# Kernel optimization log

Measured on AMD Instinct MI355X. Metric: run time of the kernel, lower is better.

## Reference

```python
import jax, jax.numpy as jnp
import numpy as np

N_NODES = 100000
N_EDGES = 800000
IN = 128
HID = 128
EMB = 64
OUT = 8
N_GRAPHS = 64


def setup_inputs() -> dict:
    key = jax.random.key(0)
    ks = jax.random.split(key, 12)
    x = jax.random.normal(ks[0], (N_NODES, IN), dtype=jnp.float32)
    edge_index = jax.random.randint(ks[1], (2, N_EDGES), 0, N_NODES, dtype=jnp.int64)
    batch = jnp.sort(jax.random.randint(ks[2], (N_NODES,), 0, N_GRAPHS, dtype=jnp.int64))
    embed = jax.random.normal(ks[3], (N_GRAPHS, EMB), dtype=jnp.float32)
    s_in = 1.0 / np.sqrt(IN).astype(np.float32)
    s_h = 1.0 / np.sqrt(HID).astype(np.float32)
    s_l = 1.0 / np.sqrt(HID + EMB).astype(np.float32)
    return {
        "x": x,
        "edge_index": edge_index,
        "batch": batch,
        "embed": embed,
        # SAGEConv1: out = lin_l(mean_agg) + lin_r(x); bias lives in lin_l
        "W1l": jax.random.normal(ks[4], (HID, IN), dtype=jnp.float32) * s_in,
        "b1l": jnp.zeros((HID,), dtype=jnp.float32),
        "W1r": jax.random.normal(ks[5], (HID, IN), dtype=jnp.float32) * s_in,
        # SAGEConv2
        "W2l": jax.random.normal(ks[6], (HID, HID), dtype=jnp.float32) * s_h,
        "b2l": jnp.zeros((HID,), dtype=jnp.float32),
        "W2r": jax.random.normal(ks[7], (HID, HID), dtype=jnp.float32) * s_h,
        # final Linear(hidden + embed_dim, out)
        "Wlin": jax.random.normal(ks[8], (OUT, HID + EMB), dtype=jnp.float32) * s_l,
        "blin": jnp.zeros((OUT,), dtype=jnp.float32),
    }


def _segment_mean(vals, idx, num_segments):
    # scatter-mean with count clamped to 1 (matches PyG scatter 'mean')
    s = jax.ops.segment_sum(vals, idx, num_segments=num_segments)
    c = jax.ops.segment_sum(jnp.ones((vals.shape[0], 1), vals.dtype), idx,
                            num_segments=num_segments)
    return s / jnp.maximum(c, 1.0)


def reference(x, edge_index, batch, embed, W1l, b1l, W1r, W2l, b2l, W2r, Wlin, blin):
    src, dst = edge_index[0], edge_index[1]

    def sage(h, Wl, bl, Wr):
        # gather source features, mean-aggregate at destination, then linear
        agg = _segment_mean(h[src], dst, N_NODES)          # [N, d]
        return agg @ Wl.T + bl + h @ Wr.T                   # [N, HID]

    h = jax.nn.relu(sage(x, W1l, b1l, W1r))
    h = jax.nn.relu(sage(h, W2l, b2l, W2r))
    pooled = _segment_mean(h, batch, N_GRAPHS)              # [G, HID]
    z = jnp.concatenate([pooled, embed], axis=1)            # [G, HID+EMB]
    return z @ Wlin.T + blin                                # [G, OUT]
```

## Files before the change

### kernel.cpp

```cpp
#include <hip/hip_runtime.h>
#include <stdint.h>

#define FEAT   128
#define GR     64
#define LDA    136
#define NBUCK  256
#define BSHIFT 9

typedef __attribute__((ext_vector_type(8))) short bf8_t;
typedef __attribute__((ext_vector_type(4))) float f4_t;

__device__ inline float bf2f(ushort h){
    union { uint u; float f; } v; v.u = ((uint)h) << 16; return v.f;
}
__device__ inline float bf2f_lo(uint u){
    union { uint u; float f; } v; v.u = u << 16; return v.f;
}
__device__ inline float bf2f_hi(uint u){
    union { uint u; float f; } v; v.u = u & 0xffff0000u; return v.f;
}
__device__ inline ushort f2bf(float f){
    union { float f; uint u; } v; v.f = f;
    uint r = (v.u + 0x7FFFu + ((v.u >> 16) & 1u)) >> 16;
    return (ushort)r;
}

__global__ void k_cast(const float* __restrict__ x, ushort* __restrict__ xb, int n4){
    int i = blockIdx.x * blockDim.x + threadIdx.x;
    if (i >= n4) return;
    float4 v = ((const float4*)x)[i];
    ushort4 o; o.x = f2bf(v.x); o.y = f2bf(v.y); o.z = f2bf(v.z); o.w = f2bf(v.w);
    ((ushort4*)xb)[i] = o;
}

__global__ void k_castw(const float* __restrict__ a0, const float* __restrict__ a1,
                        const float* __restrict__ a2, const float* __restrict__ a3,
                        ushort* __restrict__ o0, ushort* __restrict__ o1,
                        ushort* __restrict__ o2, ushort* __restrict__ o3){
    int i = blockIdx.x * blockDim.x + threadIdx.x;
    int sel = i >> 12, j = i & 4095;
    const float* s = sel == 0 ? a0 : sel == 1 ? a1 : sel == 2 ? a2 : a3;
    ushort*      d = sel == 0 ? o0 : sel == 1 ? o1 : sel == 2 ? o2 : o3;
    float4 v = ((const float4*)s)[j];
    ushort4 o; o.x = f2bf(v.x); o.y = f2bf(v.y); o.z = f2bf(v.z); o.w = f2bf(v.w);
    ((ushort4*)d)[j] = o;
}

__global__ void k_hist(const int* __restrict__ dst, int* __restrict__ bcnt, int E){
    __shared__ int h[NBUCK];
    h[threadIdx.x] = 0;
    __syncthreads();
    int base = blockIdx.x * 4096 + threadIdx.x;
    #pragma unroll
    for (int k = 0; k < 16; k++){
        int e = base + k * 256;
        if (e < E) atomicAdd(&h[dst[e] >> BSHIFT], 1);
    }
    __syncthreads();
    int c = h[threadIdx.x];
    if (c) atomicAdd(&bcnt[threadIdx.x], c);
}

__global__ void k_bscan(const int* __restrict__ bcnt, int* __restrict__ bbase,
                        int* __restrict__ bpos, int* __restrict__ rowp,
                        int* __restrict__ csr, int E, int M){
    __shared__ int sd[NBUCK];
    int t = threadIdx.x;
    int v = bcnt[t];
    sd[t] = v; __syncthreads();
    for (int off = 1; off < NBUCK; off <<= 1){
        int x = (t >= off) ? sd[t - off] : 0;
        __syncthreads();
        sd[t] += x;
        __syncthreads();
    }
    int ex = sd[t] - v;
    bbase[t] = ex;
    bpos[t]  = ex;
    if (t < 8) csr[E + t] = 0;
    if (t == NBUCK - 1){ bbase[NBUCK] = sd[t]; rowp[M] = E; }
}

__global__ __launch_bounds__(256) void k_bucket(const int* __restrict__ src,
                                                const int* __restrict__ dst,
                                                int* __restrict__ bpos,
                                                int2* __restrict__ bp, int E){
    __shared__ int h[NBUCK];
    __shared__ int bb[NBUCK];
    int t = threadIdx.x;
    h[t] = 0;
    __syncthreads();
    int base = blockIdx.x * 4096 + t;
    int bk[16], sv[16], dv[16];
    #pragma unroll
    for (int k = 0; k < 16; k++){
        int e = base + k * 256;
        if (e < E){
            dv[k] = dst[e]; sv[k] = src[e];
            bk[k] = dv[k] >> BSHIFT;
            atomicAdd(&h[bk[k]], 1);
        } else bk[k] = -1;
    }
    __syncthreads();
    int c = h[t];
    bb[t] = c ? atomicAdd(&bpos[t], c) : 0;
    __syncthreads();
    h[t] = 0;
    __syncthreads();
    #pragma unroll
    for (int k = 0; k < 16; k++){
        if (bk[k] >= 0){
            int r = atomicAdd(&h[bk[k]], 1);
            bp[bb[bk[k]] + r] = make_int2(sv[k], dv[k]);
        }
    }
}

__global__ __launch_bounds__(512) void k_csr(const int2* __restrict__ bp,
                                             const int* __restrict__ bbase,
                                             int* __restrict__ rowp,
                                             int* __restrict__ csr, int M){
    __shared__ int cnt[512];
    __shared__ int sd[512];
    int b = blockIdx.x, t = threadIdx.x;
    int nbase = b << BSHIFT;
    int nnodes = min(512, M - nbase);
    int e0 = bbase[b], e1 = bbase[b + 1];
    cnt[t] = 0;
    __syncthreads();
    for (int e = e0 + t; e < e1; e += 512)
        atomicAdd(&cnt[bp[e].y - nbase], 1);
    __syncthreads();
    int v = cnt[t];
    sd[t] = v; __syncthreads();
    for (int off = 1; off < 512; off <<= 1){
        int x = (t >= off) ? sd[t - off] : 0;
        __syncthreads();
        sd[t] += x;
        __syncthreads();
    }
    int ex = sd[t] - v;
    if (t < nnodes) rowp[nbase + t] = e0 + ex;
    cnt[t] = ex;
    __syncthreads();
    for (int e = e0 + t; e < e1; e += 512){
        int2 pr = bp[e];
        int r = atomicAdd(&cnt[pr.y - nbase], 1);
        csr[e0 + r] = pr.x;
    }
}

#define ACC4(vv)                                   \
    acc0 += bf2f_lo((vv).x); acc1 += bf2f_hi((vv).x); \
    acc2 += bf2f_lo((vv).y); acc3 += bf2f_hi((vv).y); \
    acc4 += bf2f_lo((vv).z); acc5 += bf2f_hi((vv).z); \
    acc6 += bf2f_lo((vv).w); acc7 += bf2f_hi((vv).w);

__global__ __launch_bounds__(256) void k_agg(const ushort* __restrict__ srcf,
                                             const int* __restrict__ rowp,
                                             const int* __restrict__ csr,
                                             ushort* __restrict__ aggb, int M){
    int node = blockIdx.x * 16 + (threadIdx.x >> 4);
    int l    = threadIdx.x & 15;
    if (node >= M) return;
    int s = rowp[node], e = rowp[node + 1];
    const char* base = (const char*)srcf + (uint)l * 16u;
    float acc0 = 0.f, acc1 = 0.f, acc2 = 0.f, acc3 = 0.f;
    float acc4 = 0.f, acc5 = 0.f, acc6 = 0.f, acc7 = 0.f;
    int i = s;
    for (; i + 4 <= e; i += 4){
        int idx[4];
        __builtin_memcpy(idx, csr + i, 16);
        uint4 v0 = *(const uint4*)(base + ((uint)idx[0] << 8));
        uint4 v1 = *(const uint4*)(base + ((uint)idx[1] << 8));
        uint4 v2 = *(const uint4*)(base + ((uint)idx[2] << 8));
        uint4 v3 = *(const uint4*)(base + ((uint)idx[3] << 8));
        ACC4(v0); ACC4(v1); ACC4(v2); ACC4(v3);
    }
    for (; i < e; i++){
        uint4 v = *(const uint4*)(base + ((uint)csr[i] << 8));
        ACC4(v);
    }
    float inv = (e > s) ? 1.0f / (float)(e - s) : 0.f;
    uint4 o;
    o.x = ((uint)f2bf(acc1 * inv) << 16) | (uint)f2bf(acc0 * inv);
    o.y = ((uint)f2bf(acc3 * inv) << 16) | (uint)f2bf(acc2 * inv);
    o.z = ((uint)f2bf(acc5 * inv) << 16) | (uint)f2bf(acc4 * inv);
    o.w = ((uint)f2bf(acc7 * inv) << 16) | (uint)f2bf(acc6 * inv);
    *(uint4*)(aggb + (size_t)node * FEAT + l * 8) = o;
}

__global__ __launch_bounds__(256) void k_gemm(
    const ushort* __restrict__ Aagg, const ushort* __restrict__ Aself,
    const ushort* __restrict__ Wl, const ushort* __restrict__ Wr,
    const float* __restrict__ bias, ushort* __restrict__ Hout, int M)
{
    __shared__ ushort As[64 * LDA];
    __shared__ ushort Bs[128 * LDA];
    const int tid  = threadIdx.x;
    const int lane = tid & 63;
    const int wave = tid >> 6;
    const int l15  = lane & 15;
    const int quad = lane >> 4;
    const int m0   = blockIdx.x * 64;

    f4_t acc[8];
    #pragma unroll
    for (int i = 0; i < 8; i++) acc[i] = (f4_t){0.f, 0.f, 0.f, 0.f};

    #pragma unroll
    for (int pass = 0; pass < 2; pass++){
        const ushort* Ap = pass ? Aself : Aagg;
        const ushort* Wp = pass ? Wr    : Wl;
        #pragma unroll
        for (int it = 0; it < 4; it++){
            int idx = (it * 256 + tid) * 8;
            int r = idx >> 7, c = idx & 127;
            int4 v = {0, 0, 0, 0};
            if (m0 + r < M) v = *(const int4*)(Ap + (size_t)(m0 + r) * FEAT + c);
            *(int4*)(&As[r * LDA + c]) = v;
        }
        #pragma unroll
        for (int it = 0; it < 8; it++){
            int idx = (it * 256 + tid) * 8;
            int r = idx >> 7, c = idx & 127;
            *(int4*)(&Bs[r * LDA + c]) = *(const int4*)(Wp + idx);
        }
        __syncthreads();
        const ushort* arow = &As[(wave * 16 + l15) * LDA + quad * 8];
        const ushort* brow = &Bs[l15 * LDA + quad * 8];
        #pragma unroll
        for (int nt = 0; nt < 8; nt++){
            #pragma unroll
            for (int ks = 0; ks < 4; ks++){
                bf8_t a = *(const bf8_t*)(arow + ks * 32);
                bf8_t b = *(const bf8_t*)(brow + nt * 16 * LDA + ks * 32);
                acc[nt] = __builtin_amdgcn_mfma_f32_16x16x32_bf16(a, b, acc[nt], 0, 0, 0);
            }
        }
        __syncthreads();
    }
    #pragma unroll
    for (int nt = 0; nt < 8; nt++){
        int col = nt * 16 + l15;
        float bcol = bias[col];
        #pragma unroll
        for (int reg = 0; reg < 4; reg++){
            int gm = m0 + wave * 16 + quad * 4 + reg;
            if (gm < M){
                float v = acc[nt][reg] + bcol;
                v = v > 0.f ? v : 0.f;
                Hout[(size_t)gm * FEAT + col] = f2bf(v);
            }
        }
    }
}

__global__ void k_pool(const ushort* __restrict__ h, const int* __restrict__ batch,
                       float* __restrict__ pooled, int M){
    int f   = threadIdx.x & 127;
    int sub = threadIdx.x >> 7;
    int n0  = (blockIdx.x * 2 + sub) * 16;
    if (n0 >= M) return;
    int n1 = min(n0 + 16, M);
    int g = batch[n0];
    float s = 0.f;
    int n = n0;
    for (; n + 4 <= n1; n += 4){
        int g0 = batch[n], g1 = batch[n + 1], g2 = batch[n + 2], g3 = batch[n + 3];
        float v0 = bf2f(h[(size_t)n * FEAT + f]);
        float v1 = bf2f(h[(size_t)(n + 1) * FEAT + f]);
        float v2 = bf2f(h[(size_t)(n + 2) * FEAT + f]);
        float v3 = bf2f(h[(size_t)(n + 3) * FEAT + f]);
        if (g0 != g){ atomicAdd(&pooled[g * FEAT + f], s); s = 0.f; g = g0; } s += v0;
        if (g1 != g){ atomicAdd(&pooled[g * FEAT + f], s); s = 0.f; g = g1; } s += v1;
        if (g2 != g){ atomicAdd(&pooled[g * FEAT + f], s); s = 0.f; g = g2; } s += v2;
        if (g3 != g){ atomicAdd(&pooled[g * FEAT + f], s); s = 0.f; g = g3; } s += v3;
    }
    for (; n < n1; n++){
        int gn = batch[n];
        if (gn != g){ atomicAdd(&pooled[g * FEAT + f], s); s = 0.f; g = gn; }
        s += bf2f(h[(size_t)n * FEAT + f]);
    }
    atomicAdd(&pooled[g * FEAT + f], s);
}

__global__ void k_final(const float* __restrict__ pooled, const int* __restrict__ batch,
                        const float* __restrict__ embed, const float* __restrict__ Wlin,
                        const float* __restrict__ blin, float* __restrict__ out, int M){
    int t = threadIdx.x;
    if (t >= GR * 8) return;
    int g = t >> 3, o = t & 7;
    int lo = 0, hi = M;
    while (lo < hi){ int mid = (lo + hi) >> 1; if (batch[mid] < g) lo = mid + 1; else hi = mid; }
    int s0 = lo;
    lo = s0; hi = M;
    while (lo < hi){ int mid = (lo + hi) >> 1; if (batch[mid] < g + 1) lo = mid + 1; else hi = mid; }
    int c = lo - s0;
    float inv = (c > 0) ? 1.0f / (float)c : 0.f;
    float acc = blin[o];
    const float* wr = Wlin + o * (FEAT + GR);
    for (int k = 0; k < FEAT; k++) acc += pooled[g * FEAT + k] * inv * wr[k];
    for (int k = 0; k < GR; k++)   acc += embed[g * GR + k] * wr[FEAT + k];
    out[g * 8 + o] = acc;
}

extern "C" void kernel_launch(void* const* d_in, const int* in_sizes, int n_in,
                              void* d_out, int out_size, void* d_ws, size_t ws_size,
                              hipStream_t stream)
{
    const float* x     = (const float*)d_in[0];
    const int*   eidx  = (const int*)d_in[1];
    const int*   batch = (const int*)d_in[2];
    const float* embed = (const float*)d_in[3];
    const float* W1l   = (const float*)d_in[4];
    const float* b1l   = (const float*)d_in[5];
    const float* W1r   = (const float*)d_in[6];
    const float* W2l   = (const float*)d_in[7];
    const float* b2l   = (const float*)d_in[8];
    const float* W2r   = (const float*)d_in[9];
    const float* Wlin  = (const float*)d_in[10];
    const float* blin  = (const float*)d_in[11];
    float* out = (float*)d_out;

    const int M = in_sizes[0] / FEAT;
    const int E = in_sizes[1] / 2;
    const int* src = eidx;
    const int* dst = eidx + E;

    char* w = (char*)d_ws;
    size_t off = 0;
    auto alloc = [&](size_t sz){ void* p = w + off; off = (off + sz + 255) & ~(size_t)255; return p; };
    ushort* xb     = (ushort*)alloc((size_t)M * FEAT * 2);
    ushort* aggb   = (ushort*)alloc((size_t)M * FEAT * 2);
    ushort* h1b    = (ushort*)alloc((size_t)M * FEAT * 2);
    int*    rowp   = (int*)alloc((size_t)(M + 1) * 4);
    int*    csr    = (int*)alloc((size_t)(E + 8) * 4);
    int*    bcnt   = (int*)alloc(NBUCK * 4);
    int*    bbase  = (int*)alloc((NBUCK + 1) * 4);
    int*    bpos   = (int*)alloc(NBUCK * 4);
    float*  pooled = (float*)alloc((size_t)GR * FEAT * 4);
    ushort* w1lb   = (ushort*)alloc((size_t)FEAT * FEAT * 2);
    ushort* w1rb   = (ushort*)alloc((size_t)FEAT * FEAT * 2);
    ushort* w2lb   = (ushort*)alloc((size_t)FEAT * FEAT * 2);
    ushort* w2rb   = (ushort*)alloc((size_t)FEAT * FEAT * 2);
    int2*   bp     = (int2*)aggb;
    ushort* h2b    = xb;

    hipMemsetAsync(bcnt, 0, NBUCK * 4, stream);
    hipMemsetAsync(pooled, 0, (size_t)GR * FEAT * 4, stream);

    const int nb   = (M + 511) >> BSHIFT;
    const int ebk  = (E + 4095) / 4096;
    k_cast  <<<(M * FEAT / 4 + 255) / 256, 256, 0, stream>>>(x, xb, M * FEAT / 4);
    k_castw <<<64, 256, 0, stream>>>(W1l, W1r, W2l, W2r, w1lb, w1rb, w2lb, w2rb);
    k_hist  <<<ebk, 256, 0, stream>>>(dst, bcnt, E);
    k_bscan <<<1, NBUCK, 0, stream>>>(bcnt, bbase, bpos, rowp, csr, E, M);
    k_bucket<<<ebk, 256, 0, stream>>>(src, dst, bpos, bp, E);
    k_csr   <<<nb, 512, 0, stream>>>(bp, bbase, rowp, csr, M);
    k_agg   <<<(M + 15) / 16, 256, 0, stream>>>(xb, rowp, csr, aggb, M);
    k_gemm  <<<(M + 63) / 64, 256, 0, stream>>>(aggb, xb, w1lb, w1rb, b1l, h1b, M);
    k_agg   <<<(M + 15) / 16, 256, 0, stream>>>(h1b, rowp, csr, aggb, M);
    k_gemm  <<<(M + 63) / 64, 256, 0, stream>>>(aggb, h1b, w2lb, w2rb, b2l, h2b, M);
    k_pool  <<<(M + 31) / 32, 256, 0, stream>>>(h2b, batch, pooled, M);
    k_final <<<1, 512, 0, stream>>>(pooled, batch, embed, Wlin, blin, out, M);
}
```

Measured before the change: 309.0 us.

## Fuse neighbor aggregation into SAGE GEMM kernel and read weights directly

Merges the gather-mean aggregation and the dual GEMM into one kernel per layer. Each block aggregates neighbors for its 64 rows straight into shared memory, loads self-features directly into registers, and reads weight fragments from global memory (L2-cached) instead of staging them in LDS. This removes the aggregated-feature buffer's write and re-read, plus two kernel launches per layer. In exchange, the gather phase now runs at the GEMM kernel's occupancy with one barrier before the MFMAs, and the weight loads are uncoalesced global reads.

```diff
diff --git a/kernel.cpp b/kernel.cpp
--- a/kernel.cpp
+++ b/kernel.cpp
@@ -156,47 +156,13 @@
     acc4 += bf2f_lo((vv).z); acc5 += bf2f_hi((vv).z); \
     acc6 += bf2f_lo((vv).w); acc7 += bf2f_hi((vv).w);
 
-__global__ __launch_bounds__(256) void k_agg(const ushort* __restrict__ srcf,
-                                             const int* __restrict__ rowp,
-                                             const int* __restrict__ csr,
-                                             ushort* __restrict__ aggb, int M){
-    int node = blockIdx.x * 16 + (threadIdx.x >> 4);
-    int l    = threadIdx.x & 15;
-    if (node >= M) return;
-    int s = rowp[node], e = rowp[node + 1];
-    const char* base = (const char*)srcf + (uint)l * 16u;
-    float acc0 = 0.f, acc1 = 0.f, acc2 = 0.f, acc3 = 0.f;
-    float acc4 = 0.f, acc5 = 0.f, acc6 = 0.f, acc7 = 0.f;
-    int i = s;
-    for (; i + 4 <= e; i += 4){
-        int idx[4];
-        __builtin_memcpy(idx, csr + i, 16);
-        uint4 v0 = *(const uint4*)(base + ((uint)idx[0] << 8));
-        uint4 v1 = *(const uint4*)(base + ((uint)idx[1] << 8));
-        uint4 v2 = *(const uint4*)(base + ((uint)idx[2] << 8));
-        uint4 v3 = *(const uint4*)(base + ((uint)idx[3] << 8));
-        ACC4(v0); ACC4(v1); ACC4(v2); ACC4(v3);
-    }
-    for (; i < e; i++){
-        uint4 v = *(const uint4*)(base + ((uint)csr[i] << 8));
-        ACC4(v);
-    }
-    float inv = (e > s) ? 1.0f / (float)(e - s) : 0.f;
-    uint4 o;
-    o.x = ((uint)f2bf(acc1 * inv) << 16) | (uint)f2bf(acc0 * inv);
-    o.y = ((uint)f2bf(acc3 * inv) << 16) | (uint)f2bf(acc2 * inv);
-    o.z = ((uint)f2bf(acc5 * inv) << 16) | (uint)f2bf(acc4 * inv);
-    o.w = ((uint)f2bf(acc7 * inv) << 16) | (uint)f2bf(acc6 * inv);
-    *(uint4*)(aggb + (size_t)node * FEAT + l * 8) = o;
-}
-
-__global__ __launch_bounds__(256) void k_gemm(
-    const ushort* __restrict__ Aagg, const ushort* __restrict__ Aself,
-    const ushort* __restrict__ Wl, const ushort* __restrict__ Wr,
-    const float* __restrict__ bias, ushort* __restrict__ Hout, int M)
+__global__ __launch_bounds__(256) void k_sage(
+    const ushort* __restrict__ Aself, const int* __restrict__ rowp,
+    const int* __restrict__ csr, const ushort* __restrict__ Wl,
+    const ushort* __restrict__ Wr, const float* __restrict__ bias,
+    ushort* __restrict__ Hout, int M)
 {
     __shared__ ushort As[64 * LDA];
-    __shared__ ushort Bs[128 * LDA];
     const int tid  = threadIdx.x;
     const int lane = tid & 63;
     const int wave = tid >> 6;
@@ -204,42 +170,80 @@
     const int quad = lane >> 4;
     const int m0   = blockIdx.x * 64;
 
+    int srowi = m0 + wave * 16 + l15;
+    if (srowi >= M) srowi = M - 1;
+    const ushort* srow = Aself + (size_t)srowi * FEAT + quad * 8;
+    bf8_t sa0 = *(const bf8_t*)(srow);
+    bf8_t sa1 = *(const bf8_t*)(srow + 32);
+    bf8_t sa2 = *(const bf8_t*)(srow + 64);
+    bf8_t sa3 = *(const bf8_t*)(srow + 96);
+
+    {
+        const int l   = tid & 15;
+        const int grp = tid >> 4;
+        const char* gbase = (const char*)Aself + (uint)l * 16u;
+        #pragma unroll
+        for (int p = 0; p < 4; p++){
+            int r = p * 16 + grp;
+            int node = m0 + r;
+            float acc0 = 0.f, acc1 = 0.f, acc2 = 0.f, acc3 = 0.f;
+            float acc4 = 0.f, acc5 = 0.f, acc6 = 0.f, acc7 = 0.f;
+            float inv = 0.f;
+            if (node < M){
+                int s = rowp[node], e = rowp[node + 1];
+                int i = s;
+                for (; i + 4 <= e; i += 4){
+                    int idx[4];
+                    __builtin_memcpy(idx, csr + i, 16);
+                    uint4 v0 = *(const uint4*)(gbase + ((uint)idx[0] << 8));
+                    uint4 v1 = *(const uint4*)(gbase + ((uint)idx[1] << 8));
+                    uint4 v2 = *(const uint4*)(gbase + ((uint)idx[2] << 8));
+                    uint4 v3 = *(const uint4*)(gbase + ((uint)idx[3] << 8));
+                    ACC4(v0); ACC4(v1); ACC4(v2); ACC4(v3);
+                }
+                for (; i < e; i++){
+                    uint4 v = *(const uint4*)(gbase + ((uint)csr[i] << 8));
+                    ACC4(v);
+                }
+                inv = (e > s) ? 1.0f / (float)(e - s) : 0.f;
+            }
+            uint4 o;
+            o.x = ((uint)f2bf(acc1 * inv) << 16) | (uint)f2bf(acc0 * inv);
+            o.y = ((uint)f2bf(acc3 * inv) << 16) | (uint)f2bf(acc2 * inv);
+            o.z = ((uint)f2bf(acc5 * inv) << 16) | (uint)f2bf(acc4 * inv);
+            o.w = ((uint)f2bf(acc7 * inv) << 16) | (uint)f2bf(acc6 * inv);
+            *(uint4*)(&As[r * LDA + l * 8]) = o;
+        }
+    }
+    __syncthreads();
+
     f4_t acc[8];
     #pragma unroll
     for (int i = 0; i < 8; i++) acc[i] = (f4_t){0.f, 0.f, 0.f, 0.f};
 
-    #pragma unroll
-    for (int pass = 0; pass < 2; pass++){
-        const ushort* Ap = pass ? Aself : Aagg;
-        const ushort* Wp = pass ? Wr    : Wl;
-        #pragma unroll
-        for (int it = 0; it < 4; it++){
-            int idx = (it * 256 + tid) * 8;
-            int r = idx >> 7, c = idx & 127;
-            int4 v = {0, 0, 0, 0};
-            if (m0 + r < M) v = *(const int4*)(Ap + (size_t)(m0 + r) * FEAT + c);
-            *(int4*)(&As[r * LDA + c]) = v;
-        }
-        #pragma unroll
-        for (int it = 0; it < 8; it++){
-            int idx = (it * 256 + tid) * 8;
-            int r = idx >> 7, c = idx & 127;
-            *(int4*)(&Bs[r * LDA + c]) = *(const int4*)(Wp + idx);
-        }
-        __syncthreads();
-        const ushort* arow = &As[(wave * 16 + l15) * LDA + quad * 8];
-        const ushort* brow = &Bs[l15 * LDA + quad * 8];
-        #pragma unroll
-        for (int nt = 0; nt < 8; nt++){
-            #pragma unroll
-            for (int ks = 0; ks < 4; ks++){
-                bf8_t a = *(const bf8_t*)(arow + ks * 32);
-                bf8_t b = *(const bf8_t*)(brow + nt * 16 * LDA + ks * 32);
-                acc[nt] = __builtin_amdgcn_mfma_f32_16x16x32_bf16(a, b, acc[nt], 0, 0, 0);
-            }
-        }
-        __syncthreads();
-    }
+    const ushort* agrow = &As[(wave * 16 + l15) * LDA + quad * 8];
+    bf8_t ga0 = *(const bf8_t*)(agrow);
+    bf8_t ga1 = *(const bf8_t*)(agrow + 32);
+    bf8_t ga2 = *(const bf8_t*)(agrow + 64);
+    bf8_t ga3 = *(const bf8_t*)(agrow + 96);
+
+    #pragma unroll
+    for (int nt = 0; nt < 8; nt++){
+        const ushort* wl = Wl + (size_t)(nt * 16 + l15) * FEAT + quad * 8;
+        acc[nt] = __builtin_amdgcn_mfma_f32_16x16x32_bf16(ga0, *(const bf8_t*)(wl),      acc[nt], 0, 0, 0);
+        acc[nt] = __builtin_amdgcn_mfma_f32_16x16x32_bf16(ga1, *(const bf8_t*)(wl + 32), acc[nt], 0, 0, 0);
+        acc[nt] = __builtin_amdgcn_mfma_f32_16x16x32_bf16(ga2, *(const bf8_t*)(wl + 64), acc[nt], 0, 0, 0);
+        acc[nt] = __builtin_amdgcn_mfma_f32_16x16x32_bf16(ga3, *(const bf8_t*)(wl + 96), acc[nt], 0, 0, 0);
+    }
+    #pragma unroll
+    for (int nt = 0; nt < 8; nt++){
+        const ushort* wr = Wr + (size_t)(nt * 16 + l15) * FEAT + quad * 8;
+        acc[nt] = __builtin_amdgcn_mfma_f32_16x16x32_bf16(sa0, *(const bf8_t*)(wr),      acc[nt], 0, 0, 0);
+        acc[nt] = __builtin_amdgcn_mfma_f32_16x16x32_bf16(sa1, *(const bf8_t*)(wr + 32), acc[nt], 0, 0, 0);
+        acc[nt] = __builtin_amdgcn_mfma_f32_16x16x32_bf16(sa2, *(const bf8_t*)(wr + 64), acc[nt], 0, 0, 0);
+        acc[nt] = __builtin_amdgcn_mfma_f32_16x16x32_bf16(sa3, *(const bf8_t*)(wr + 96), acc[nt], 0, 0, 0);
+    }
+
     #pragma unroll
     for (int nt = 0; nt < 8; nt++){
         int col = nt * 16 + l15;
@@ -332,7 +336,6 @@
     size_t off = 0;
     auto alloc = [&](size_t sz){ void* p = w + off; off = (off + sz + 255) & ~(size_t)255; return p; };
     ushort* xb     = (ushort*)alloc((size_t)M * FEAT * 2);
-    ushort* aggb   = (ushort*)alloc((size_t)M * FEAT * 2);
     ushort* h1b    = (ushort*)alloc((size_t)M * FEAT * 2);
     int*    rowp   = (int*)alloc((size_t)(M + 1) * 4);
     int*    csr    = (int*)alloc((size_t)(E + 8) * 4);
@@ -344,7 +347,7 @@
     ushort* w1rb   = (ushort*)alloc((size_t)FEAT * FEAT * 2);
     ushort* w2lb   = (ushort*)alloc((size_t)FEAT * FEAT * 2);
     ushort* w2rb   = (ushort*)alloc((size_t)FEAT * FEAT * 2);
-    int2*   bp     = (int2*)aggb;
+    int2*   bp     = (int2*)h1b;
     ushort* h2b    = xb;
 
     hipMemsetAsync(bcnt, 0, NBUCK * 4, stream);
@@ -358,10 +361,8 @@
     k_bscan <<<1, NBUCK, 0, stream>>>(bcnt, bbase, bpos, rowp, csr, E, M);
     k_bucket<<<ebk, 256, 0, stream>>>(src, dst, bpos, bp, E);
     k_csr   <<<nb, 512, 0, stream>>>(bp, bbase, rowp, csr, M);
-    k_agg   <<<(M + 15) / 16, 256, 0, stream>>>(xb, rowp, csr, aggb, M);
-    k_gemm  <<<(M + 63) / 64, 256, 0, stream>>>(aggb, xb, w1lb, w1rb, b1l, h1b, M);
-    k_agg   <<<(M + 15) / 16, 256, 0, stream>>>(h1b, rowp, csr, aggb, M);
-    k_gemm  <<<(M + 63) / 64, 256, 0, stream>>>(aggb, h1b, w2lb, w2rb, b2l, h2b, M);
+    k_sage  <<<(M + 63) / 64, 256, 0, stream>>>(xb,  rowp, csr, w1lb, w1rb, b1l, h1b, M);
+    k_sage  <<<(M + 63) / 64, 256, 0, stream>>>(h1b, rowp, csr, w2lb, w2rb, b2l, h2b, M);
     k_pool  <<<(M + 31) / 32, 256, 0, stream>>>(h2b, batch, pooled, M);
     k_final <<<1, 512, 0, stream>>>(pooled, batch, embed, Wlin, blin, out, M);
 }
```

Result: slower. 384.2 us (+24.3%).

## Unroll gather aggregation to 8 edges; load GEMM A operands directly into registers

Applied to the files above, without the earlier changes.

The aggregation kernel now issues 8 independent neighbor-row loads per iteration and splits the sums across two accumulator sets, to raise memory-level parallelism on the random gather. The GEMM kernel drops the shared-memory staging of the activation tile: each lane loads its MFMA A fragments straight from global memory, which removes LDS traffic and shrinks the shared allocation. Out-of-range rows are clamped to the last valid row instead of zero-filled, which is harmless because the store is still masked. The cost is higher register pressure in both kernels.

```diff
diff --git a/kernel.cpp b/kernel.cpp
--- a/kernel.cpp
+++ b/kernel.cpp
@@ -150,11 +150,16 @@
     }
 }
 
-#define ACC4(vv)                                   \
-    acc0 += bf2f_lo((vv).x); acc1 += bf2f_hi((vv).x); \
-    acc2 += bf2f_lo((vv).y); acc3 += bf2f_hi((vv).y); \
-    acc4 += bf2f_lo((vv).z); acc5 += bf2f_hi((vv).z); \
-    acc6 += bf2f_lo((vv).w); acc7 += bf2f_hi((vv).w);
+#define ACCA(vv)                                   \
+    a0 += bf2f_lo((vv).x); a1 += bf2f_hi((vv).x);  \
+    a2 += bf2f_lo((vv).y); a3 += bf2f_hi((vv).y);  \
+    a4 += bf2f_lo((vv).z); a5 += bf2f_hi((vv).z);  \
+    a6 += bf2f_lo((vv).w); a7 += bf2f_hi((vv).w);
+#define ACCB(vv)                                   \
+    b0 += bf2f_lo((vv).x); b1 += bf2f_hi((vv).x);  \
+    b2 += bf2f_lo((vv).y); b3 += bf2f_hi((vv).y);  \
+    b4 += bf2f_lo((vv).z); b5 += bf2f_hi((vv).z);  \
+    b6 += bf2f_lo((vv).w); b7 += bf2f_hi((vv).w);
 
 __global__ __launch_bounds__(256) void k_agg(const ushort* __restrict__ srcf,
                                              const int* __restrict__ rowp,
@@ -165,28 +170,45 @@
     if (node >= M) return;
     int s = rowp[node], e = rowp[node + 1];
     const char* base = (const char*)srcf + (uint)l * 16u;
-    float acc0 = 0.f, acc1 = 0.f, acc2 = 0.f, acc3 = 0.f;
-    float acc4 = 0.f, acc5 = 0.f, acc6 = 0.f, acc7 = 0.f;
+    float a0 = 0.f, a1 = 0.f, a2 = 0.f, a3 = 0.f;
+    float a4 = 0.f, a5 = 0.f, a6 = 0.f, a7 = 0.f;
+    float b0 = 0.f, b1 = 0.f, b2 = 0.f, b3 = 0.f;
+    float b4 = 0.f, b5 = 0.f, b6 = 0.f, b7 = 0.f;
     int i = s;
-    for (; i + 4 <= e; i += 4){
+    for (; i + 8 <= e; i += 8){
+        int idx[8];
+        __builtin_memcpy(idx, csr + i, 32);
+        uint4 v0 = *(const uint4*)(base + ((uint)idx[0] << 8));
+        uint4 v1 = *(const uint4*)(base + ((uint)idx[1] << 8));
+        uint4 v2 = *(const uint4*)(base + ((uint)idx[2] << 8));
+        uint4 v3 = *(const uint4*)(base + ((uint)idx[3] << 8));
+        uint4 v4 = *(const uint4*)(base + ((uint)idx[4] << 8));
+        uint4 v5 = *(const uint4*)(base + ((uint)idx[5] << 8));
+        uint4 v6 = *(const uint4*)(base + ((uint)idx[6] << 8));
+        uint4 v7 = *(const uint4*)(base + ((uint)idx[7] << 8));
+        ACCA(v0); ACCA(v1); ACCA(v2); ACCA(v3);
+        ACCB(v4); ACCB(v5); ACCB(v6); ACCB(v7);
+    }
+    if (i + 4 <= e){
         int idx[4];
         __builtin_memcpy(idx, csr + i, 16);
         uint4 v0 = *(const uint4*)(base + ((uint)idx[0] << 8));
         uint4 v1 = *(const uint4*)(base + ((uint)idx[1] << 8));
         uint4 v2 = *(const uint4*)(base + ((uint)idx[2] << 8));
         uint4 v3 = *(const uint4*)(base + ((uint)idx[3] << 8));
-        ACC4(v0); ACC4(v1); ACC4(v2); ACC4(v3);
+        ACCA(v0); ACCA(v1); ACCB(v2); ACCB(v3);
+        i += 4;
     }
     for (; i < e; i++){
         uint4 v = *(const uint4*)(base + ((uint)csr[i] << 8));
-        ACC4(v);
+        ACCA(v);
     }
     float inv = (e > s) ? 1.0f / (float)(e - s) : 0.f;
     uint4 o;
-    o.x = ((uint)f2bf(acc1 * inv) << 16) | (uint)f2bf(acc0 * inv);
-    o.y = ((uint)f2bf(acc3 * inv) << 16) | (uint)f2bf(acc2 * inv);
-    o.z = ((uint)f2bf(acc5 * inv) << 16) | (uint)f2bf(acc4 * inv);
-    o.w = ((uint)f2bf(acc7 * inv) << 16) | (uint)f2bf(acc6 * inv);
+    o.x = ((uint)f2bf((a1 + b1) * inv) << 16) | (uint)f2bf((a0 + b0) * inv);
+    o.y = ((uint)f2bf((a3 + b3) * inv) << 16) | (uint)f2bf((a2 + b2) * inv);
+    o.z = ((uint)f2bf((a5 + b5) * inv) << 16) | (uint)f2bf((a4 + b4) * inv);
+    o.w = ((uint)f2bf((a7 + b7) * inv) << 16) | (uint)f2bf((a6 + b6) * inv);
     *(uint4*)(aggb + (size_t)node * FEAT + l * 8) = o;
 }
 
@@ -195,7 +217,6 @@
     const ushort* __restrict__ Wl, const ushort* __restrict__ Wr,
     const float* __restrict__ bias, ushort* __restrict__ Hout, int M)
 {
-    __shared__ ushort As[64 * LDA];
     __shared__ ushort Bs[128 * LDA];
     const int tid  = threadIdx.x;
     const int lane = tid & 63;
@@ -204,39 +225,38 @@
     const int quad = lane >> 4;
     const int m0   = blockIdx.x * 64;
 
+    int arow = m0 + wave * 16 + l15;
+    if (arow >= M) arow = M - 1;
+    const ushort* ap0 = Aagg  + (size_t)arow * FEAT + quad * 8;
+    const ushort* ap1 = Aself + (size_t)arow * FEAT + quad * 8;
+
     f4_t acc[8];
     #pragma unroll
     for (int i = 0; i < 8; i++) acc[i] = (f4_t){0.f, 0.f, 0.f, 0.f};
 
     #pragma unroll
     for (int pass = 0; pass < 2; pass++){
-        const ushort* Ap = pass ? Aself : Aagg;
-        const ushort* Wp = pass ? Wr    : Wl;
-        #pragma unroll
-        for (int it = 0; it < 4; it++){
-            int idx = (it * 256 + tid) * 8;
-            int r = idx >> 7, c = idx & 127;
-            int4 v = {0, 0, 0, 0};
-            if (m0 + r < M) v = *(const int4*)(Ap + (size_t)(m0 + r) * FEAT + c);
-            *(int4*)(&As[r * LDA + c]) = v;
-        }
+        const ushort* Ap = pass ? ap1 : ap0;
+        const ushort* Wp = pass ? Wr  : Wl;
         #pragma unroll
         for (int it = 0; it < 8; it++){
             int idx = (it * 256 + tid) * 8;
             int r = idx >> 7, c = idx & 127;
             *(int4*)(&Bs[r * LDA + c]) = *(const int4*)(Wp + idx);
         }
-        __syncthreads();
-        const ushort* arow = &As[(wave * 16 + l15) * LDA + quad * 8];
+        bf8_t ga0 = *(const bf8_t*)(Ap);
+        bf8_t ga1 = *(const bf8_t*)(Ap + 32);
+        bf8_t ga2 = *(const bf8_t*)(Ap + 64);
+        bf8_t ga3 = *(const bf8_t*)(Ap + 96);
+        __syncthreads();
         const ushort* brow = &Bs[l15 * LDA + quad * 8];
         #pragma unroll
         for (int nt = 0; nt < 8; nt++){
-            #pragma unroll
-            for (int ks = 0; ks < 4; ks++){
-                bf8_t a = *(const bf8_t*)(arow + ks * 32);
-                bf8_t b = *(const bf8_t*)(brow + nt * 16 * LDA + ks * 32);
-                acc[nt] = __builtin_amdgcn_mfma_f32_16x16x32_bf16(a, b, acc[nt], 0, 0, 0);
-            }
+            const ushort* b = brow + nt * 16 * LDA;
+            acc[nt] = __builtin_amdgcn_mfma_f32_16x16x32_bf16(ga0, *(const bf8_t*)(b),      acc[nt], 0, 0, 0);
+            acc[nt] = __builtin_amdgcn_mfma_f32_16x16x32_bf16(ga1, *(const bf8_t*)(b + 32), acc[nt], 0, 0, 0);
+            acc[nt] = __builtin_amdgcn_mfma_f32_16x16x32_bf16(ga2, *(const bf8_t*)(b + 64), acc[nt], 0, 0, 0);
+            acc[nt] = __builtin_amdgcn_mfma_f32_16x16x32_bf16(ga3, *(const bf8_t*)(b + 96), acc[nt], 0, 0, 0);
         }
         __syncthreads();
     }
```

Measured after the change: 306.1 us. No clear change (-0.9%).
